# Optimization experiments

Hardware: AMD Instinct MI355X
Metric: run time of the kernel (lower is better)

## Reference

```python
import jax, jax.numpy as jnp
import numpy as np

VOCAB = 50257
K = 10  # accuracy_slack_size


def setup_inputs() -> dict:
    key = jax.random.key(0)
    k1, k2, k3, k4 = jax.random.split(key, 4)
    logits = jax.random.normal(k1, (4, 2048, 512), dtype=jnp.float32)
    target = jax.random.randint(k2, (4, 2048), 0, VOCAB, dtype=jnp.int64 if jax.config.jax_enable_x64 else jnp.int32)
    mask = jax.random.randint(k3, (4, 2048), 0, 2, dtype=jnp.int32)
    W = jax.random.normal(k4, (512, VOCAB), dtype=jnp.float32) * 0.02
    b = jnp.zeros((VOCAB,), dtype=jnp.float32)
    return {"logits": logits, "target": target, "mask": mask, "W": W, "b": b}


def reference(logits, target, mask, W, b):
    N = logits.shape[0] * logits.shape[1]
    x = logits.reshape(N, logits.shape[-1])            # [N, d]
    # sampled_softmax.log_prob: full log-softmax over vocab
    logp = jax.nn.log_softmax(x @ W + b, axis=-1)      # [N, V]
    _, words = jax.lax.top_k(logp, K)                  # [N, K] indices
    tgt = target.reshape(-1)                           # [N]
    msk = mask.reshape(-1).astype(jnp.float32)         # [N]
    # vectorized membership: is target among top-K predictions?
    hit = jnp.any(words == tgt[:, None], axis=1).astype(jnp.float32)
    counter = jnp.sum(hit * msk)
    all_counter = jnp.sum(msk)
    return jnp.array([counter / all_counter])
```

## Files before the change

### kernel.cpp

```cpp
#include <hip/hip_runtime.h>
#include <stdint.h>

#define V_VOCAB 50257
#define V_PAD   50432
#define NT_N    197
#define NROWS   8192
#define DIM     512
#define KTOP    10
#define MARGIN  0.3f
#define ACH     8

typedef __attribute__((ext_vector_type(8))) short  short8;
typedef __attribute__((ext_vector_type(4))) float  f32x4;

struct Ctrl { int mc; int namb; int hits; int pad_; };

#define OFF_WT     0ULL
#define SZ_WT      51642368ULL
#define OFF_XC     (OFF_WT + SZ_WT)
#define SZ_XC      8388608ULL
#define OFF_BPAD   (OFF_XC + SZ_XC)
#define SZ_BPAD    (50432ULL*4)
#define OFF_ROWIDX (OFF_BPAD + SZ_BPAD)
#define OFF_THAT   (OFF_ROWIDX + 32768ULL)
#define OFF_COUNTS (OFF_THAT + 32768ULL)
#define OFF_AMB    (OFF_COUNTS + 32768ULL)
#define OFF_CTRL   (OFF_AMB + 32768ULL)
#define OFF_RK     (OFF_CTRL + 16ULL)
#define OFF_SST    (OFF_RK + 32768ULL)

#define GLOAD16(gp, lp) __builtin_amdgcn_global_load_lds( \
    (const __attribute__((address_space(1))) unsigned int*)(gp), \
    (__attribute__((address_space(3))) unsigned int*)(lp), 16, 0, 0)

#define SBAR()  do { asm volatile("" ::: "memory"); __builtin_amdgcn_s_barrier(); \
                     asm volatile("" ::: "memory"); } while (0)
#define LGKM0() asm volatile("s_waitcnt lgkmcnt(0)" ::: "memory")
#define VM2()   asm volatile("s_waitcnt vmcnt(2)" ::: "memory")
#define VM0()   asm volatile("s_waitcnt vmcnt(0)" ::: "memory")

__device__ __forceinline__ unsigned short f2bf(float f) {
  unsigned int u = __builtin_bit_cast(unsigned int, f);
  unsigned int r = (u + 0x7FFFu + ((u >> 16) & 1u)) >> 16;
  return (unsigned short)r;
}
__device__ __forceinline__ float bf2f(unsigned short h) {
  unsigned int u = ((unsigned int)h) << 16;
  return __builtin_bit_cast(float, u);
}

__global__ void k_prep(const int* __restrict__ mask, const float* __restrict__ b,
                       float* __restrict__ bpad, int* __restrict__ rowidx,
                       Ctrl* __restrict__ ctrl) {
  int i = blockIdx.x * 256 + threadIdx.x;
  if (i < V_PAD) bpad[i] = (i < V_VOCAB) ? b[i] : -1e30f;
  if (i < NROWS && mask[i] != 0) {
    int p = atomicAdd(&ctrl->mc, 1);
    rowidx[p] = i;
  }
}

__global__ void k_twt(const float* __restrict__ W, unsigned short* __restrict__ Wt) {
  __shared__ float lt[64][65];
  const int vbase = blockIdx.x * 64;
  const int kbase = blockIdx.y * 64;
  const int tid = threadIdx.x;
  const int krow = tid >> 6;
  const int col  = tid & 63;
  const int v    = vbase + col;
#pragma unroll
  for (int rr = 0; rr < 16; ++rr) {
    int kl = krow + rr * 4;
    float val = (v < V_VOCAB) ? W[(size_t)(kbase + kl) * V_VOCAB + v] : 0.0f;
    lt[kl][col] = val;
  }
  __syncthreads();
  const int vr = tid >> 3;
  const int kc = tid & 7;
#pragma unroll
  for (int p = 0; p < 2; ++p) {
    int vl = p * 32 + vr;
    short8 t;
#pragma unroll
    for (int j = 0; j < 8; ++j) t[j] = (short)f2bf(lt[kc * 8 + j][vl]);
    *(short8*)(Wt + (size_t)(vbase + vl) * DIM + kbase + kc * 8) = t;
  }
}

__global__ void k_xc(const float* __restrict__ x, const int* __restrict__ rowidx,
                     const Ctrl* __restrict__ ctrl, unsigned short* __restrict__ Xc) {
  const int wid = threadIdx.x >> 6, lane = threadIdx.x & 63;
  const int i = blockIdx.x * 4 + wid;
  const int mc = ctrl->mc;
  short8 t;
  if (i < mc) {
    const float* src = x + (size_t)rowidx[i] * DIM + lane * 8;
#pragma unroll
    for (int j = 0; j < 8; ++j) t[j] = (short)f2bf(src[j]);
  } else {
#pragma unroll
    for (int j = 0; j < 8; ++j) t[j] = 0;
  }
  *(short8*)(Xc + (size_t)i * DIM + lane * 8) = t;
}

__global__ void k_that(const unsigned short* __restrict__ Xc,
                       const unsigned short* __restrict__ Wt,
                       const float* __restrict__ bpad,
                       const int* __restrict__ rowidx, const int* __restrict__ target,
                       const Ctrl* __restrict__ ctrl, float* __restrict__ that) {
  const int wid = threadIdx.x >> 6, lane = threadIdx.x & 63;
  const int i = blockIdx.x * 4 + wid;
  const int mc = ctrl->mc;
  if (i >= mc) { if (lane == 0) that[i] = 1e30f; return; }
  const int tg = target[rowidx[i]];
  short8 xa = *(const short8*)(Xc + (size_t)i * DIM + lane * 8);
  short8 wa = *(const short8*)(Wt + (size_t)tg * DIM + lane * 8);
  float s = 0.f;
#pragma unroll
  for (int j = 0; j < 8; ++j)
    s += bf2f((unsigned short)xa[j]) * bf2f((unsigned short)wa[j]);
#pragma unroll
  for (int d = 1; d < 64; d <<= 1) s += __shfl_xor(s, d, 64);
  if (lane == 0) that[i] = s + bpad[tg];
}

__launch_bounds__(512, 2)
__global__ void k_count(const unsigned short* __restrict__ Xc,
                        const unsigned short* __restrict__ Wt,
                        const float* __restrict__ bpad, const float* __restrict__ that,
                        const Ctrl* __restrict__ ctrl, unsigned int* __restrict__ counts) {
  const int mc = ctrl->mc;
  const int lin = blockIdx.y * NT_N + blockIdx.x;
  const int wg  = (lin & 7) * 788 + (lin >> 3);
  const int mt = wg & 31;
  const int nt = wg >> 5;
  const int mbase = mt * 256;
  if (mbase >= mc) return;
  const int nbase = nt * 256;

  __shared__ char lds[131072];

  const int tid  = threadIdx.x;
  const int lane = tid & 63;
  const int w    = tid >> 6;
  const int wr   = w >> 2;
  const int wc   = w & 3;

  const char* Ag = (const char*)Xc + (size_t)mbase * 1024;
  const char* Bg = (const char*)Wt + (size_t)nbase * 1024;
  const int s2 = (tid & 7) ^ ((tid >> 3) & 7);
  const size_t gsrc_off = (size_t)(tid >> 3) * 1024 + (size_t)s2 * 16;
  const int    ldst_off = (tid >> 3) * 128 + (tid & 7) * 16;

#define STAGE_HALF(isA, q, h, ktb) do {                                        \
    const char* _g = ((isA) ? Ag : Bg) + (size_t)(h) * 131072 + (size_t)(ktb) + gsrc_off; \
    char* _l = lds + ((isA) ? 0 : 65536) + (q) * 32768 + (h) * 16384 + ldst_off; \
    GLOAD16(_g, _l);                                                           \
    GLOAD16(_g + 65536, _l + 8192);                                            \
  } while (0)

  const int fr = lane & 15;
  const int fq = lane >> 4;
  const int sl0 = (fq)     ^ (lane & 7);
  const int sl1 = (4 + fq) ^ (lane & 7);

#define LDA4(q, ks, mh) do {                                                   \
    const char* _b = lds + (q) * 32768;                                        \
    const int _sl = (ks) ? sl1 : sl0;                                          \
    _Pragma("unroll") for (int _j = 0; _j < 4; ++_j) {                         \
      const int _r = wr * 128 + (mh) * 64 + _j * 16 + fr;                      \
      af[_j] = *(const short8*)(_b + _r * 128 + _sl * 16); }                   \
  } while (0)
#define LDB4(q, ks) do {                                                       \
    const char* _b = lds + 65536 + (q) * 32768;                                \
    const int _sl = (ks) ? sl1 : sl0;                                          \
    _Pragma("unroll") for (int _j = 0; _j < 4; ++_j) {                         \
      const int _r = wc * 64 + _j * 16 + fr;                                   \
      bf[_j] = *(const short8*)(_b + _r * 128 + _sl * 16); }                   \
  } while (0)
#define MFMA16(mh) do {                                                        \
    __builtin_amdgcn_s_setprio(1);                                             \
    _Pragma("unroll") for (int _m = 0; _m < 4; ++_m)                           \
    _Pragma("unroll") for (int _n = 0; _n < 4; ++_n)                           \
      acc[(mh) * 4 + _m][_n] = __builtin_amdgcn_mfma_f32_16x16x32_bf16(        \
          af[_m], bf[_n], acc[(mh) * 4 + _m][_n], 0, 0, 0);                    \
    __builtin_amdgcn_s_setprio(0);                                             \
  } while (0)

  f32x4 acc[8][4];
#pragma unroll
  for (int a = 0; a < 8; ++a)
#pragma unroll
    for (int c = 0; c < 4; ++c) acc[a][c] = (f32x4)0.0f;

  short8 af[4], bf[4];

  STAGE_HALF(0, 0, 0, 0);   STAGE_HALF(0, 0, 1, 0);
  STAGE_HALF(1, 0, 0, 0);   STAGE_HALF(1, 0, 1, 0);
  STAGE_HALF(0, 1, 0, 128);
  VM2(); SBAR();

#pragma unroll
  for (int i = 0; i < 4; ++i) {
    const int ktn  = (2 * i + 1) * 128;
    const int ktp2 = (2 * i + 2 < 8 ? 2 * i + 2 : 0) * 128;
    const int ktp3 = (2 * i + 3 < 8 ? 2 * i + 3 : 0) * 128;
    LDB4(0, 0); LDA4(0, 0, 0);
    STAGE_HALF(0, 1, 1, ktn);
    SBAR(); LGKM0(); MFMA16(0); SBAR();
    LDA4(0, 0, 1);
    STAGE_HALF(1, 1, 0, ktn);
    SBAR(); LGKM0(); MFMA16(1); SBAR();
    LDB4(0, 1); LDA4(0, 1, 0);
    STAGE_HALF(1, 1, 1, ktn);
    SBAR(); LGKM0(); MFMA16(0); SBAR();
    LDA4(0, 1, 1);
    STAGE_HALF(0, 0, 0, ktp2);
    SBAR(); LGKM0(); MFMA16(1);
    VM2(); SBAR();
    LDB4(1, 0); LDA4(1, 0, 0);
    STAGE_HALF(0, 0, 1, ktp2);
    SBAR(); LGKM0(); MFMA16(0); SBAR();
    LDA4(1, 0, 1);
    STAGE_HALF(1, 0, 0, ktp2);
    SBAR(); LGKM0(); MFMA16(1); SBAR();
    LDB4(1, 1); LDA4(1, 1, 0);
    STAGE_HALF(1, 0, 1, ktp2);
    SBAR(); LGKM0(); MFMA16(0); SBAR();
    LDA4(1, 1, 1);
    STAGE_HALF(0, 1, 0, ktp3);
    SBAR(); LGKM0(); MFMA16(1);
    VM2(); SBAR();
  }
  VM0();

  float bv[4];
#pragma unroll
  for (int ni = 0; ni < 4; ++ni)
    bv[ni] = bpad[nbase + wc * 64 + ni * 16 + fr];

#pragma unroll
  for (int mi = 0; mi < 8; ++mi) {
#pragma unroll
    for (int r = 0; r < 4; ++r) {
      const int m = mbase + wr * 128 + mi * 16 + fq * 4 + r;
      const float th  = that[m];
      const float tlo = th - MARGIN, thi = th + MARGIN;
      unsigned int p = 0;
#pragma unroll
      for (int ni = 0; ni < 4; ++ni) {
        const float s = acc[mi][ni][r] + bv[ni];
        p += (s > tlo) ? 1u : 0u;
        p += (s > thi) ? (1u << 16) : 0u;
      }
      int pi = (int)p;
#pragma unroll
      for (int d = 1; d < 16; d <<= 1) pi += __shfl_xor(pi, d, 64);
      if ((lane & 15) == 0) atomicAdd(&counts[m], (unsigned int)pi);
    }
  }
#undef STAGE_HALF
#undef LDA4
#undef LDB4
#undef MFMA16
}

__global__ void k_decide(const unsigned int* __restrict__ counts,
                         Ctrl* __restrict__ ctrl, int* __restrict__ amb) {
  const int i = blockIdx.x * 256 + threadIdx.x;
  if (i >= ctrl->mc) return;
  const unsigned int c = counts[i];
  const unsigned int lo = c & 0xFFFFu, hi = c >> 16;
  if (lo <= KTOP - 1) { atomicAdd(&ctrl->hits, 1); }
  else if (hi >= KTOP) {  }
  else { int p = atomicAdd(&ctrl->namb, 1); amb[p] = i; }
}

__global__ void k_fixt(const float* __restrict__ x, const float* __restrict__ W,
                       const float* __restrict__ b, const int* __restrict__ rowidx,
                       const int* __restrict__ target, const int* __restrict__ amb,
                       const Ctrl* __restrict__ ctrl, float* __restrict__ sst) {
  const int a = blockIdx.x * 64 + threadIdx.x;
  if (a >= ctrl->namb) return;
  const int n = rowidx[amb[a]];
  const int tg = target[n];
  float st = 0.f;
  for (int k = 0; k < DIM; ++k)
    st = fmaf(x[(size_t)n * DIM + k], W[(size_t)k * V_VOCAB + tg], st);
  sst[a] = st + b[tg];
}

__global__ void k_fixscan(const float* __restrict__ x, const float* __restrict__ W,
                          const float* __restrict__ b, const int* __restrict__ rowidx,
                          const int* __restrict__ target, const int* __restrict__ amb,
                          const float* __restrict__ sst, const Ctrl* __restrict__ ctrl,
                          int* __restrict__ rk) {
  __shared__ float sx[ACH][DIM];
  const int j = blockIdx.x * 256 + threadIdx.x;
  const int namb = ctrl->namb;
  const float bj = (j < V_VOCAB) ? b[j] : 0.f;
  for (int base = 0; base < namb; base += ACH) {
    __syncthreads();
    for (int t = threadIdx.x; t < ACH * DIM / 4; t += 256) {
      const int a  = t / (DIM / 4);
      const int kk = (t % (DIM / 4)) * 4;
      f32x4 v = (f32x4)0.f;
      if (base + a < namb) {
        const int n = rowidx[amb[base + a]];
        v = *(const f32x4*)(x + (size_t)n * DIM + kk);
      }
      *(f32x4*)(&sx[a][kk]) = v;
    }
    __syncthreads();
    if (j >= V_VOCAB) continue;
    float s[ACH];
#pragma unroll
    for (int a = 0; a < ACH; ++a) s[a] = 0.f;
    for (int k = 0; k < DIM; ++k) {
      const float wv = W[(size_t)k * V_VOCAB + j];
#pragma unroll
      for (int a = 0; a < ACH; ++a) s[a] = fmaf(sx[a][k], wv, s[a]);
    }
#pragma unroll
    for (int a = 0; a < ACH; ++a) {
      if (base + a < namb) {
        const int tg = target[rowidx[amb[base + a]]];
        const float sc = s[a] + bj;
        const float st = sst[base + a];
        if (sc > st || (sc == st && j < tg)) atomicAdd(&rk[base + a], 1);
      }
    }
  }
}

__global__ void k_fixdec(const int* __restrict__ rk, Ctrl* __restrict__ ctrl) {
  const int a = blockIdx.x * 256 + threadIdx.x;
  if (a < ctrl->namb && rk[a] <= KTOP - 1) atomicAdd(&ctrl->hits, 1);
}

__global__ void k_final(const Ctrl* __restrict__ ctrl, float* __restrict__ out) {
  out[0] = (float)ctrl->hits / (float)ctrl->mc;
}

extern "C" void kernel_launch(void* const* d_in, const int* in_sizes, int n_in,
                              void* d_out, int out_size, void* d_ws, size_t ws_size,
                              hipStream_t stream) {
  const float* x      = (const float*)d_in[0];
  const int*   target = (const int*)d_in[1];
  const int*   mask   = (const int*)d_in[2];
  const float* W      = (const float*)d_in[3];
  const float* b      = (const float*)d_in[4];
  float* out = (float*)d_out;

  char* ws = (char*)d_ws;
  unsigned short* Wt     = (unsigned short*)(ws + OFF_WT);
  unsigned short* Xc     = (unsigned short*)(ws + OFF_XC);
  float*          bpad   = (float*)(ws + OFF_BPAD);
  int*            rowidx = (int*)(ws + OFF_ROWIDX);
  float*          that   = (float*)(ws + OFF_THAT);
  unsigned int*   counts = (unsigned int*)(ws + OFF_COUNTS);
  int*            amb    = (int*)(ws + OFF_AMB);
  Ctrl*           ctrl   = (Ctrl*)(ws + OFF_CTRL);
  int*            rk     = (int*)(ws + OFF_RK);
  float*          sst    = (float*)(ws + OFF_SST);

  hipMemsetAsync(ws + OFF_COUNTS, 0, 32768 + 32768 + 16 + 32768, stream);

  k_prep   <<<197, 256, 0, stream>>>(mask, b, bpad, rowidx, ctrl);
  k_twt    <<<dim3(788, 8), 256, 0, stream>>>(W, Wt);
  k_xc     <<<2048, 256, 0, stream>>>(x, rowidx, ctrl, Xc);
  k_that   <<<2048, 256, 0, stream>>>(Xc, Wt, bpad, rowidx, target, ctrl, that);
  k_count  <<<dim3(NT_N, 32), 512, 0, stream>>>(Xc, Wt, bpad, that, ctrl, counts);
  k_decide <<<32, 256, 0, stream>>>(counts, ctrl, amb);
  k_fixt   <<<128, 64, 0, stream>>>(x, W, b, rowidx, target, amb, ctrl, sst);
  k_fixscan<<<197, 256, 0, stream>>>(x, W, b, rowidx, target, amb, sst, ctrl, rk);
  k_fixdec <<<32, 256, 0, stream>>>(rk, ctrl);
  k_final  <<<1, 1, 0, stream>>>(ctrl, out);
}
```

Baseline: 518.1 us.

## Make k_count a persistent kernel that prefetches the next tile across tiles

Replaces the 2D grid of one-tile workgroups with 256 persistent workgroups that loop over the active M×N tiles with a stride of 256. The first K-slices of the next tile are staged into LDS while the last slices of the current tile are still being computed, so the pipeline prologue and launch cost are paid once per workgroup instead of once per tile. This also drops early-exit blocks for inactive M tiles. In exchange, the tile order changes from the old swizzle to M-fastest, which may change L2 reuse of W, and the epilogue now sits on the critical path between tiles.

After: 527.9 us. About the same (+1.9%).

```diff
diff --git a/kernel.cpp b/kernel.cpp
--- a/kernel.cpp
+++ b/kernel.cpp
@@ -131,13 +131,11 @@
                         const float* __restrict__ bpad, const float* __restrict__ that,
                         const Ctrl* __restrict__ ctrl, unsigned int* __restrict__ counts) {
   const int mc = ctrl->mc;
-  const int lin = blockIdx.y * NT_N + blockIdx.x;
-  const int wg  = (lin & 7) * 788 + (lin >> 3);
-  const int mt = wg & 31;
-  const int nt = wg >> 5;
-  const int mbase = mt * 256;
-  if (mbase >= mc) return;
-  const int nbase = nt * 256;
+  const int amt = (mc + 255) >> 8;
+  const int ntiles = amt * NT_N;
+  const int bid = blockIdx.x;
+  if (bid >= ntiles) return;
+  const int nj = (ntiles - bid + 255) >> 8;
 
   __shared__ char lds[131072];
 
@@ -147,17 +145,21 @@
   const int wr   = w >> 2;
   const int wc   = w & 3;
 
-  const char* Ag = (const char*)Xc + (size_t)mbase * 1024;
-  const char* Bg = (const char*)Wt + (size_t)nbase * 1024;
   const int s2 = (tid & 7) ^ ((tid >> 3) & 7);
   const size_t gsrc_off = (size_t)(tid >> 3) * 1024 + (size_t)s2 * 16;
   const int    ldst_off = (tid >> 3) * 128 + (tid & 7) * 16;
 
-#define STAGE_HALF(isA, q, h, ktb) do {                                        \
-    const char* _g = ((isA) ? Ag : Bg) + (size_t)(h) * 131072 + (size_t)(ktb) + gsrc_off; \
-    char* _l = lds + ((isA) ? 0 : 65536) + (q) * 32768 + (h) * 16384 + ldst_off; \
-    GLOAD16(_g, _l);                                                           \
-    GLOAD16(_g + 65536, _l + 8192);                                            \
+#define STAGE_A(q, h, gb, ktb) do {                                           \
+    const char* _g = (gb) + (size_t)(h) * 131072 + (size_t)(ktb) + gsrc_off;  \
+    char* _l = lds + (q) * 32768 + (h) * 16384 + ldst_off;                    \
+    GLOAD16(_g, _l);                                                          \
+    GLOAD16(_g + 65536, _l + 8192);                                           \
+  } while (0)
+#define STAGE_B(q, h, gb, ktb) do {                                           \
+    const char* _g = (gb) + (size_t)(h) * 131072 + (size_t)(ktb) + gsrc_off;  \
+    char* _l = lds + 65536 + (q) * 32768 + (h) * 16384 + ldst_off;            \
+    GLOAD16(_g, _l);                                                          \
+    GLOAD16(_g + 65536, _l + 8192);                                           \
   } while (0)
 
   const int fr = lane & 15;
@@ -196,71 +198,96 @@
 
   short8 af[4], bf[4];
 
-  STAGE_HALF(0, 0, 0, 0);   STAGE_HALF(0, 0, 1, 0);
-  STAGE_HALF(1, 0, 0, 0);   STAGE_HALF(1, 0, 1, 0);
-  STAGE_HALF(0, 1, 0, 128);
+  int t = bid;
+  int mi = t % amt, nt = t / amt;
+  const char* Ag = (const char*)Xc + ((size_t)mi << 18);
+  const char* Bg = (const char*)Wt + ((size_t)nt << 18);
+
+  STAGE_B(0, 0, Bg, 0);   STAGE_B(0, 1, Bg, 0);
+  STAGE_A(0, 0, Ag, 0);   STAGE_A(0, 1, Ag, 0);
+  STAGE_B(1, 0, Bg, 128);
   VM2(); SBAR();
 
-#pragma unroll
-  for (int i = 0; i < 4; ++i) {
-    const int ktn  = (2 * i + 1) * 128;
-    const int ktp2 = (2 * i + 2 < 8 ? 2 * i + 2 : 0) * 128;
-    const int ktp3 = (2 * i + 3 < 8 ? 2 * i + 3 : 0) * 128;
-    LDB4(0, 0); LDA4(0, 0, 0);
-    STAGE_HALF(0, 1, 1, ktn);
-    SBAR(); LGKM0(); MFMA16(0); SBAR();
-    LDA4(0, 0, 1);
-    STAGE_HALF(1, 1, 0, ktn);
-    SBAR(); LGKM0(); MFMA16(1); SBAR();
-    LDB4(0, 1); LDA4(0, 1, 0);
-    STAGE_HALF(1, 1, 1, ktn);
-    SBAR(); LGKM0(); MFMA16(0); SBAR();
-    LDA4(0, 1, 1);
-    STAGE_HALF(0, 0, 0, ktp2);
-    SBAR(); LGKM0(); MFMA16(1);
-    VM2(); SBAR();
-    LDB4(1, 0); LDA4(1, 0, 0);
-    STAGE_HALF(0, 0, 1, ktp2);
-    SBAR(); LGKM0(); MFMA16(0); SBAR();
-    LDA4(1, 0, 1);
-    STAGE_HALF(1, 0, 0, ktp2);
-    SBAR(); LGKM0(); MFMA16(1); SBAR();
-    LDB4(1, 1); LDA4(1, 1, 0);
-    STAGE_HALF(1, 0, 1, ktp2);
-    SBAR(); LGKM0(); MFMA16(0); SBAR();
-    LDA4(1, 1, 1);
-    STAGE_HALF(0, 1, 0, ktp3);
-    SBAR(); LGKM0(); MFMA16(1);
-    VM2(); SBAR();
+  for (int j = 0; j < nj; ++j) {
+    const int t1  = (j == nj - 1) ? t : t + 256;
+    const int mi1 = t1 % amt, nt1 = t1 / amt;
+    const char* AgN = (const char*)Xc + ((size_t)mi1 << 18);
+    const char* BgN = (const char*)Wt + ((size_t)nt1 << 18);
+
+#pragma unroll
+    for (int i = 0; i < 4; ++i) {
+      const int ktn = (2 * i + 1) * 128;
+      const char* A2 = (i < 3) ? Ag : AgN;
+      const char* B2 = (i < 3) ? Bg : BgN;
+      const int kt2 = (i < 3) ? (2 * i + 2) * 128 : 0;
+      const int kt3 = (i < 3) ? (2 * i + 3) * 128 : 128;
+      LDB4(0, 0); LDA4(0, 0, 0);
+      STAGE_B(1, 1, Bg, ktn);
+      SBAR(); LGKM0(); MFMA16(0); SBAR();
+      LDA4(0, 0, 1);
+      STAGE_A(1, 0, Ag, ktn);
+      SBAR(); LGKM0(); MFMA16(1); SBAR();
+      LDB4(0, 1); LDA4(0, 1, 0);
+      STAGE_A(1, 1, Ag, ktn);
+      SBAR(); LGKM0(); MFMA16(0); SBAR();
+      LDA4(0, 1, 1);
+      STAGE_B(0, 0, B2, kt2);
+      SBAR(); LGKM0(); MFMA16(1);
+      VM2(); SBAR();
+      LDB4(1, 0); LDA4(1, 0, 0);
+      STAGE_B(0, 1, B2, kt2);
+      SBAR(); LGKM0(); MFMA16(0); SBAR();
+      LDA4(1, 0, 1);
+      STAGE_A(0, 0, A2, kt2);
+      SBAR(); LGKM0(); MFMA16(1); SBAR();
+      LDB4(1, 1); LDA4(1, 1, 0);
+      STAGE_A(0, 1, A2, kt2);
+      SBAR(); LGKM0(); MFMA16(0); SBAR();
+      LDA4(1, 1, 1);
+      STAGE_B(1, 0, B2, kt3);
+      SBAR(); LGKM0(); MFMA16(1);
+      VM2(); SBAR();
+    }
+
+    {
+      const int nbase = nt << 8;
+      const int mbase = mi << 8;
+      float bv[4];
+#pragma unroll
+      for (int ni = 0; ni < 4; ++ni)
+        bv[ni] = bpad[nbase + wc * 64 + ni * 16 + fr];
+
+#pragma unroll
+      for (int fi = 0; fi < 8; ++fi) {
+#pragma unroll
+        for (int r = 0; r < 4; ++r) {
+          const int m = mbase + wr * 128 + fi * 16 + fq * 4 + r;
+          const float th  = that[m];
+          const float tlo = th - MARGIN, thi = th + MARGIN;
+          unsigned int p = 0;
+#pragma unroll
+          for (int ni = 0; ni < 4; ++ni) {
+            const float s = acc[fi][ni][r] + bv[ni];
+            p += (s > tlo) ? 1u : 0u;
+            p += (s > thi) ? (1u << 16) : 0u;
+          }
+          int pi = (int)p;
+#pragma unroll
+          for (int d = 1; d < 16; d <<= 1) pi += __shfl_xor(pi, d, 64);
+          if ((lane & 15) == 0) atomicAdd(&counts[m], (unsigned int)pi);
+        }
+      }
+#pragma unroll
+      for (int a = 0; a < 8; ++a)
+#pragma unroll
+        for (int c = 0; c < 4; ++c) acc[a][c] = (f32x4)0.0f;
+    }
+
+    t = t1; mi = mi1; nt = nt1; Ag = AgN; Bg = BgN;
   }
   VM0();
-
-  float bv[4];
-#pragma unroll
-  for (int ni = 0; ni < 4; ++ni)
-    bv[ni] = bpad[nbase + wc * 64 + ni * 16 + fr];
-
-#pragma unroll
-  for (int mi = 0; mi < 8; ++mi) {
-#pragma unroll
-    for (int r = 0; r < 4; ++r) {
-      const int m = mbase + wr * 128 + mi * 16 + fq * 4 + r;
-      const float th  = that[m];
-      const float tlo = th - MARGIN, thi = th + MARGIN;
-      unsigned int p = 0;
-#pragma unroll
-      for (int ni = 0; ni < 4; ++ni) {
-        const float s = acc[mi][ni][r] + bv[ni];
-        p += (s > tlo) ? 1u : 0u;
-        p += (s > thi) ? (1u << 16) : 0u;
-      }
-      int pi = (int)p;
-#pragma unroll
-      for (int d = 1; d < 16; d <<= 1) pi += __shfl_xor(pi, d, 64);
-      if ((lane & 15) == 0) atomicAdd(&counts[m], (unsigned int)pi);
-    }
-  }
-#undef STAGE_HALF
+#undef STAGE_A
+#undef STAGE_B
 #undef LDA4
 #undef LDB4
 #undef MFMA16
@@ -371,7 +398,7 @@
   k_twt    <<<dim3(788, 8), 256, 0, stream>>>(W, Wt);
   k_xc     <<<2048, 256, 0, stream>>>(x, rowidx, ctrl, Xc);
   k_that   <<<2048, 256, 0, stream>>>(Xc, Wt, bpad, rowidx, target, ctrl, that);
-  k_count  <<<dim3(NT_N, 32), 512, 0, stream>>>(Xc, Wt, bpad, that, ctrl, counts);
+  k_count  <<<256, 512, 0, stream>>>(Xc, Wt, bpad, that, ctrl, counts);
   k_decide <<<32, 256, 0, stream>>>(counts, ctrl, amb);
   k_fixt   <<<128, 64, 0, stream>>>(x, W, b, rowidx, target, amb, ctrl, sst);
   k_fixscan<<<197, 256, 0, stream>>>(x, W, b, rowidx, target, amb, sst, ctrl, rk);
```
